# Kernel tuning notes

Hardware: AMD Instinct MI355X
Metric: run time of the kernel (lower is better)

## Reference

```python
import jax, jax.numpy as jnp
import numpy as np

T = 2048
HIDDEN = 4096
NH = 32        # query heads
NKV = 8        # kv heads
G = NH // NKV  # GQA group size
D = 128        # head_dim (== v_head_dim)
ROPE_BASE = 1000000.0


def setup_inputs() -> dict:
    key = jax.random.key(0)
    ks = jax.random.split(key, 8)
    s = 0.02
    return {
        "positions": jnp.arange(T, dtype=jnp.int32),
        "hidden_states": jax.random.normal(ks[0], (T, HIDDEN), dtype=jnp.float32),
        "Wq": jax.random.normal(ks[1], (HIDDEN, NH * D), dtype=jnp.float32) * s,
        "bq": jnp.zeros((NH * D,), dtype=jnp.float32),
        "Wk": jax.random.normal(ks[2], (HIDDEN, NKV * D), dtype=jnp.float32) * s,
        "bk": jnp.zeros((NKV * D,), dtype=jnp.float32),
        "Wv": jax.random.normal(ks[3], (HIDDEN, NKV * D), dtype=jnp.float32) * s,
        "bv": jnp.zeros((NKV * D,), dtype=jnp.float32),
        "Wo": jax.random.normal(ks[4], (NH * D, HIDDEN), dtype=jnp.float32) * s,
    }


def _rope(positions, x):
    # neox-style rotary, full rotary_dim = D
    half = D // 2
    inv_freq = 1.0 / (ROPE_BASE ** (jnp.arange(0, half, dtype=jnp.float32) / half))
    freqs = positions.astype(jnp.float32)[:, None] * inv_freq[None, :]  # [T, half]
    cos = jnp.cos(freqs)[:, None, :]  # [T, 1, half]
    sin = jnp.sin(freqs)[:, None, :]
    x1, x2 = x[..., :half], x[..., half:]
    return jnp.concatenate([x1 * cos - x2 * sin, x2 * cos + x1 * sin], axis=-1)


def reference(positions, hidden_states, Wq, bq, Wk, bk, Wv, bv, Wo):
    q = (hidden_states @ Wq + bq).reshape(T, NH, D)
    k = (hidden_states @ Wk + bk).reshape(T, NKV, D)
    v = (hidden_states @ Wv + bv).reshape(T, NKV, D)
    q = _rope(positions, q)
    k = _rope(positions, k)

    scale = D ** -0.5
    qg = q.reshape(T, NKV, G, D)
    # scores: [NKV, G, T(query), S(key)]
    scores = jnp.einsum("tkgd,skd->kgts", qg, k) * scale
    causal = positions[:, None] >= positions[None, :]  # [T, S]
    scores = jnp.where(causal[None, None, :, :], scores, jnp.finfo(scores.dtype).min)
    probs = jax.nn.softmax(scores, axis=-1)
    attn = jnp.einsum("kgts,skd->tkgd", probs, v).reshape(T, NH * D)

    output = attn @ Wo
    kv_fused = jnp.stack([k, v], axis=0)  # [2, T, NKV, D]
    return output, kv_fused
```

## Files before the change

### kernel.cpp

```cpp
#include <hip/hip_runtime.h>
#include <stdint.h>

#define T_SEQ 2048
#define HIDDEN_DIM 4096
#define NH 32
#define NKV 8
#define HD 128
#define QKV_N 6144

typedef unsigned short u16;
typedef __attribute__((__ext_vector_type__(8))) __bf16 bf16x8;
typedef __attribute__((__ext_vector_type__(4))) float f32x4;

__device__ __forceinline__ float exp2_fast(float x) {
    return __builtin_amdgcn_exp2f(x);
}

__device__ __forceinline__ u16 f2bf(float f) {
    union { float f; unsigned u; } x; x.f = f;
    unsigned u = x.u;
    unsigned r = u + 0x7FFFu + ((u >> 16) & 1u);
    return (u16)(r >> 16);
}
__device__ __forceinline__ float bf2f(u16 h) {
    union { unsigned u; float f; } x; x.u = ((unsigned)h) << 16;
    return x.f;
}

__device__ __forceinline__ void gl_lds16(const u16* g, u16* l) {
    __builtin_amdgcn_global_load_lds((__attribute__((address_space(1))) void*)g,
                                     (__attribute__((address_space(3))) void*)l,
                                     16, 0, 0);
}

#define BAR()                                  \
    {                                          \
        asm volatile("" ::: "memory");         \
        __builtin_amdgcn_s_barrier();          \
        asm volatile("" ::: "memory");         \
    }

template <int N>
__device__ __forceinline__ void vmwait() {
    if constexpr (N == 0) asm volatile("s_waitcnt vmcnt(0)" ::: "memory");
    else if constexpr (N == 3) asm volatile("s_waitcnt vmcnt(3)" ::: "memory");
    else if constexpr (N == 4) asm volatile("s_waitcnt vmcnt(4)" ::: "memory");
    else if constexpr (N == 6) asm volatile("s_waitcnt vmcnt(6)" ::: "memory");
    else if constexpr (N == 8) asm volatile("s_waitcnt vmcnt(8)" ::: "memory");
}

__global__ __launch_bounds__(256) void cast_f32_bf16(const float* __restrict__ in,
                                                     u16* __restrict__ out, int n4) {
    int i = blockIdx.x * 256 + threadIdx.x;
    if (i < n4) {
        float4 v = ((const float4*)in)[i];
        uint2 o;
        o.x = (unsigned)f2bf(v.x) | ((unsigned)f2bf(v.y) << 16);
        o.y = (unsigned)f2bf(v.z) | ((unsigned)f2bf(v.w) << 16);
        ((uint2*)out)[i] = o;
    }
}

__global__ __launch_bounds__(256) void transpose_cast(const float* __restrict__ W,
                                                      u16* __restrict__ Wt, int R, int C) {
    __shared__ float tile[32][33];
    int c0 = blockIdx.x * 32, r0 = blockIdx.y * 32;
    int tx = threadIdx.x & 31;
    int ty = threadIdx.x >> 5;
#pragma unroll
    for (int i = 0; i < 32; i += 8)
        tile[ty + i][tx] = W[(size_t)(r0 + ty + i) * C + c0 + tx];
    __syncthreads();
#pragma unroll
    for (int i = 0; i < 32; i += 8)
        Wt[(size_t)(c0 + ty + i) * R + r0 + tx] = f2bf(tile[tx][ty + i]);
}

__global__ __launch_bounds__(256) void concat_bias(const float* __restrict__ bq,
                                                   const float* __restrict__ bk,
                                                   const float* __restrict__ bv,
                                                   float* __restrict__ out) {
    int i = blockIdx.x * 256 + threadIdx.x;
    if (i < 4096) out[i] = bq[i];
    else if (i < 5120) out[i] = bk[i - 4096];
    else if (i < 6144) out[i] = bv[i - 5120];
}

#define STAGE(SL, S)                                                                         \
    {                                                                                        \
        const size_t ko_ = (size_t)(S) * 32;                                                 \
        _Pragma("unroll") for (int c_ = 0; c_ < ACALLS; ++c_)                                \
            gl_lds16(Ast + ko_ + (size_t)(c_ * 128) * K, &As[SL][c_ * 4096 + wave * 512]);   \
        _Pragma("unroll") for (int c_ = 0; c_ < BFULL; ++c_)                                 \
            gl_lds16(Bst + ko_ + (size_t)(c_ * 128) * K, &Bs[SL][c_ * 4096 + wave * 512]);   \
        if (BHALF) gl_lds16(BstH + ko_, &Bs[SL][BFULL * 4096 + (wave & 3) * 512]);           \
    }

#define REGION(SLOT, NSLOT, CA, CB, NA, NB, RN)                                              \
    {                                                                                        \
        if (RN) {                                                                            \
            _Pragma("unroll") for (int n_ = 0; n_ < NF; ++n_)                                \
                NB[n_] = *(const bf16x8*)&Bs[NSLOT][boff[n_]];                               \
            _Pragma("unroll") for (int m_ = 0; m_ < MF; ++m_)                                \
                NA[m_] = *(const bf16x8*)&As[NSLOT][aoff[m_]];                               \
        }                                                                                    \
        __builtin_amdgcn_s_setprio(1);                                                       \
        _Pragma("unroll") for (int m_ = 0; m_ < MF; ++m_)                                    \
            _Pragma("unroll") for (int n_ = 0; n_ < NF; ++n_)                                \
                acc[m_][n_] = __builtin_amdgcn_mfma_f32_16x16x32_bf16(CA[m_], CB[n_],        \
                                                                      acc[m_][n_], 0, 0, 0); \
        __builtin_amdgcn_s_setprio(0);                                                       \
    }

#define KSTEP(S, SLOT, STG, VMW, RN, CA, CB, NA, NB)          \
    {                                                         \
        if (STG) STAGE((((SLOT) + 3) & 3), (S) + 3)           \
        vmwait<VMW>();                                        \
        BAR();                                                \
        REGION(SLOT, (((SLOT) + 1) & 3), CA, CB, NA, NB, RN)  \
        BAR();                                                \
    }

template <int MF, int NF, int ACALLS, int BFULL, int BHALF, int BF16_OUT, int HAS_BIAS>
__global__ __launch_bounds__(512, 2) void gemm_ph(const u16* __restrict__ A,
                                                  const u16* __restrict__ Bt,
                                                  const float* __restrict__ bias,
                                                  void* __restrict__ Cv,
                                                  int M, int N, int K) {
    constexpr int BM = MF * 32;
    constexpr int BN = NF * 64;
    constexpr int LPS = ACALLS + BFULL + BHALF;
    __shared__ alignas(16) u16 As[4][BM * 32];
    __shared__ alignas(16) u16 Bs[4][BN * 32];
    const int tid = threadIdx.x;
    const int wave = tid >> 6;
    const int lane = tid & 63;
    const int l15 = lane & 15;
    const int quad = lane >> 4;
    const int wr = wave >> 2;
    const int wc = wave & 3;

    const int nbn = N / BN;
    const int q8 = (int)gridDim.x >> 3;
    const int wg = blockIdx.x;
    const int swz = (wg & 7) * q8 + (wg >> 3);
    const int m0 = (swz / nbn) * BM;
    const int n0 = (swz % nbn) * BN;

    const int srow = tid >> 2;
    const int schunk = (tid & 3) ^ ((tid >> 3) & 3);
    const u16* Ast = A + (size_t)(m0 + srow) * K + schunk * 8;
    const u16* Bst = Bt + (size_t)(n0 + srow) * K + schunk * 8;
    const int srowH = (tid & 255) >> 2;
    const u16* BstH = Bt + (size_t)(n0 + BFULL * 128 + srowH) * K + schunk * 8;

    int aoff[MF], boff[NF];
#pragma unroll
    for (int m = 0; m < MF; ++m) {
        int row = wr * (MF * 16) + m * 16 + l15;
        aoff[m] = row * 32 + ((quad ^ ((row >> 1) & 3)) << 3);
    }
#pragma unroll
    for (int n = 0; n < NF; ++n) {
        int row = wc * (NF * 16) + n * 16 + l15;
        boff[n] = row * 32 + ((quad ^ ((row >> 1) & 3)) << 3);
    }

    bf16x8 fA0[MF], fB0[NF], fA1[MF], fB1[NF];
    f32x4 acc[MF][NF] = {};
    const int NS = K >> 5;

    STAGE(0, 0) STAGE(1, 1) STAGE(2, 2)
    vmwait<LPS>();
    BAR();
#pragma unroll
    for (int n = 0; n < NF; ++n) fB0[n] = *(const bf16x8*)&Bs[0][boff[n]];
#pragma unroll
    for (int m = 0; m < MF; ++m) fA0[m] = *(const bf16x8*)&As[0][aoff[m]];

#pragma unroll 1
    for (int s = 0; s < NS - 4; s += 4) {
        KSTEP(s, 0, 1, 2 * LPS, 1, fA0, fB0, fA1, fB1)
        KSTEP(s + 1, 1, 1, 2 * LPS, 1, fA1, fB1, fA0, fB0)
        KSTEP(s + 2, 2, 1, 2 * LPS, 1, fA0, fB0, fA1, fB1)
        KSTEP(s + 3, 3, 1, 2 * LPS, 1, fA1, fB1, fA0, fB0)
    }
    {
        const int s = NS - 4;
        KSTEP(s, 0, 1, 2 * LPS, 1, fA0, fB0, fA1, fB1)
        KSTEP(s + 1, 1, 0, LPS, 1, fA1, fB1, fA0, fB0)
        KSTEP(s + 2, 2, 0, 0, 1, fA0, fB0, fA1, fB1)
        KSTEP(s + 3, 3, 0, 0, 0, fA1, fB1, fA0, fB0)
    }

#pragma unroll
    for (int m = 0; m < MF; ++m) {
        const int row = m0 + wr * (MF * 16) + m * 16 + quad * 4;
#pragma unroll
        for (int n = 0; n < NF; ++n) {
            const int col = n0 + wc * (NF * 16) + n * 16 + l15;
            float b = HAS_BIAS ? bias[col] : 0.f;
#pragma unroll
            for (int r = 0; r < 4; ++r) {
                float v = acc[m][n][r] + b;
                if (BF16_OUT) ((u16*)Cv)[(size_t)(row + r) * N + col] = f2bf(v);
                else ((float*)Cv)[(size_t)(row + r) * N + col] = v;
            }
        }
    }
}

__global__ __launch_bounds__(256) void rope_kernel(const int* __restrict__ positions,
                                                   const u16* __restrict__ qkv,
                                                   u16* __restrict__ qh,
                                                   u16* __restrict__ kh,
                                                   u16* __restrict__ vt,
                                                   float* __restrict__ kv_out) {
    const int t = blockIdx.x;
    const float pos = (float)positions[t];
    const size_t rowbase = (size_t)t * QKV_N;
    const float nlog = -13.815510557964274f / 64.f;
    const float KZ = 0.08838834764831845f * 1.4426950408889634f;
    for (int col = threadIdx.x; col < QKV_N; col += 256) {
        if (col < 4096) {
            int hh = col >> 7, d = col & 127, j = d & 63;
            float ang = pos * __expf((float)j * nlog);
            float cs = cosf(ang), sn = sinf(ang);
            size_t base = rowbase + (size_t)(col & ~127);
            float x1 = bf2f(qkv[base + j]);
            float x2 = bf2f(qkv[base + 64 + j]);
            float v = (d < 64) ? (x1 * cs - x2 * sn) : (x2 * cs + x1 * sn);
            qh[((size_t)hh * T_SEQ + t) * HD + d] = f2bf(v * KZ);
        } else if (col < 5120) {
            int lc = col - 4096, hh = lc >> 7, d = lc & 127, j = d & 63;
            float ang = pos * __expf((float)j * nlog);
            float cs = cosf(ang), sn = sinf(ang);
            size_t base = rowbase + 4096 + (size_t)hh * 128;
            float x1 = bf2f(qkv[base + j]);
            float x2 = bf2f(qkv[base + 64 + j]);
            float v = (d < 64) ? (x1 * cs - x2 * sn) : (x2 * cs + x1 * sn);
            kh[((size_t)hh * T_SEQ + t) * HD + d] = f2bf(v);
            kv_out[((size_t)t * NKV + hh) * HD + d] = v;
        } else {
            int lc = col - 5120, hh = lc >> 7, d = lc & 127;
            float v = bf2f(qkv[rowbase + 5120 + (size_t)hh * 128 + d]);
            vt[((size_t)hh * HD + d) * T_SEQ + t] = f2bf(v);
            kv_out[(((size_t)T_SEQ + t) * NKV + hh) * HD + d] = v;
        }
    }
}

#define KS_STRIDE 136
#define VS_STRIDE 72
#define PS_STRIDE 72

__global__ __launch_bounds__(256) void attn_kernel(const u16* __restrict__ Qh,
                                                   const u16* __restrict__ Kh,
                                                   const u16* __restrict__ Vt,
                                                   u16* __restrict__ attn_out) {
    __shared__ alignas(16) u16 Ks[64 * KS_STRIDE];
    __shared__ alignas(16) u16 Vs[128 * VS_STRIDE];
    __shared__ alignas(16) u16 Ps[4][32 * PS_STRIDE];

    const int h = blockIdx.y;
    const int x = blockIdx.x;
    const int zig = (x & 1) ? ((x - 1) >> 1) : (15 - (x >> 1));
    const int qb = (h < 16) ? zig : (15 - zig);
    const int tid = threadIdx.x;
    const int wave = tid >> 6;
    const int lane = tid & 63;
    const int l15 = lane & 15;
    const int quad = lane >> 4;
    const int kvh = h >> 2;
    const int wrow0 = qb * 128 + wave * 32;

    const u16* Qp = Qh + ((size_t)h * T_SEQ + wrow0) * HD;
    const u16* Kp = Kh + (size_t)kvh * T_SEQ * HD;
    const u16* Vp = Vt + (size_t)kvh * HD * T_SEQ;

    bf16x8 aQ[2][4];
#pragma unroll
    for (int i = 0; i < 2; ++i)
#pragma unroll
        for (int kb = 0; kb < 4; ++kb)
            aQ[i][kb] = *(const bf16x8*)&Qp[(size_t)(i * 16 + l15) * HD + kb * 32 + quad * 8];

    bf16x8 ones;
#pragma unroll
    for (int z = 0; z < 8; ++z) ones[z] = (__bf16)1.0f;

    f32x4 acc[2][8] = {};
    f32x4 accl[2] = {};

    const int n_tiles = 2 * qb + 2;

    const int krow = tid >> 4;
    const int kcol = (tid & 15) * 8;
    const int vrow = tid >> 3;
    const int vcol = (tid & 7) * 8;

#pragma unroll 1
    for (int t = 0; t < n_tiles; ++t) {
        const int s0 = t * 64;
        __syncthreads();
#pragma unroll
        for (int rep = 0; rep < 4; ++rep) {
            int r = krow + rep * 16;
            *(uint4*)&Ks[r * KS_STRIDE + kcol] =
                *(const uint4*)&Kp[(size_t)(s0 + r) * HD + kcol];
        }
#pragma unroll
        for (int rep = 0; rep < 4; ++rep) {
            int d = vrow + rep * 32;
            *(uint4*)&Vs[d * VS_STRIDE + vcol] =
                *(const uint4*)&Vp[(size_t)d * T_SEQ + s0 + vcol];
        }
        __syncthreads();

        if (s0 <= wrow0 + 31) {
            f32x4 sc[2][4];
#pragma unroll
            for (int j = 0; j < 4; ++j) {
                f32x4 sa = {}, sb = {};
#pragma unroll
                for (int kb = 0; kb < 4; ++kb) {
                    bf16x8 bK = *(const bf16x8*)&Ks[(j * 16 + l15) * KS_STRIDE + kb * 32 + quad * 8];
                    sa = __builtin_amdgcn_mfma_f32_16x16x32_bf16(aQ[0][kb], bK, sa, 0, 0, 0);
                    sb = __builtin_amdgcn_mfma_f32_16x16x32_bf16(aQ[1][kb], bK, sb, 0, 0, 0);
                }
                sc[0][j] = sa;
                sc[1][j] = sb;
            }
#pragma unroll
            for (int i = 0; i < 2; ++i)
#pragma unroll
                for (int r = 0; r < 4; ++r) {
                    int t_idx = wrow0 + i * 16 + quad * 4 + r;
#pragma unroll
                    for (int j = 0; j < 4; ++j) {
                        int s_idx = s0 + j * 16 + l15;
                        float z = (s_idx > t_idx) ? -1e30f : sc[i][j][r];
                        float p = exp2_fast(z);
                        Ps[wave][(i * 16 + quad * 4 + r) * PS_STRIDE + j * 16 + l15] = f2bf(p);
                    }
                }
            bf16x8 aP[2][2];
#pragma unroll
            for (int i = 0; i < 2; ++i)
#pragma unroll
                for (int k2 = 0; k2 < 2; ++k2)
                    aP[i][k2] = *(const bf16x8*)&Ps[wave][(i * 16 + l15) * PS_STRIDE + k2 * 32 + quad * 8];
#pragma unroll
            for (int o = 0; o < 8; ++o) {
                bf16x8 bV0 = *(const bf16x8*)&Vs[(o * 16 + l15) * VS_STRIDE + quad * 8];
                bf16x8 bV1 = *(const bf16x8*)&Vs[(o * 16 + l15) * VS_STRIDE + 32 + quad * 8];
#pragma unroll
                for (int i = 0; i < 2; ++i) {
                    acc[i][o] = __builtin_amdgcn_mfma_f32_16x16x32_bf16(aP[i][0], bV0, acc[i][o], 0, 0, 0);
                    acc[i][o] = __builtin_amdgcn_mfma_f32_16x16x32_bf16(aP[i][1], bV1, acc[i][o], 0, 0, 0);
                }
            }
#pragma unroll
            for (int i = 0; i < 2; ++i) {
                accl[i] = __builtin_amdgcn_mfma_f32_16x16x32_bf16(aP[i][0], ones, accl[i], 0, 0, 0);
                accl[i] = __builtin_amdgcn_mfma_f32_16x16x32_bf16(aP[i][1], ones, accl[i], 0, 0, 0);
            }
        }
    }

#pragma unroll
    for (int i = 0; i < 2; ++i)
#pragma unroll
        for (int r = 0; r < 4; ++r) {
            float inv = 1.f / accl[i][r];
            int t_idx = wrow0 + i * 16 + quad * 4 + r;
#pragma unroll
            for (int o = 0; o < 8; ++o)
                attn_out[(size_t)t_idx * (NH * HD) + h * HD + o * 16 + l15] =
                    f2bf(acc[i][o][r] * inv);
        }
}

extern "C" void kernel_launch(void* const* d_in, const int* in_sizes, int n_in,
                              void* d_out, int out_size, void* d_ws, size_t ws_size,
                              hipStream_t stream) {
    const int* positions = (const int*)d_in[0];
    const float* hidden = (const float*)d_in[1];
    const float* Wq = (const float*)d_in[2];
    const float* bq = (const float*)d_in[3];
    const float* Wk = (const float*)d_in[4];
    const float* bk = (const float*)d_in[5];
    const float* Wv = (const float*)d_in[6];
    const float* bv = (const float*)d_in[7];
    const float* Wo = (const float*)d_in[8];

    char* ws = (char*)d_ws;
    u16* hs_bf   = (u16*)(ws + 0);
    u16* attnbuf = (u16*)(ws + 0);
    u16* wqkvT   = (u16*)(ws + 16777216);
    u16* woT     = (u16*)(ws + 16777216);
    u16* qkvbuf  = (u16*)(ws + 67108864);
    u16* qbuf    = (u16*)(ws + 92274688);
    u16* kbuf    = (u16*)(ws + 109051904);
    u16* vtbuf   = (u16*)(ws + 113246208);
    float* biasb = (float*)(ws + 117440512);

    float* out0 = (float*)d_out;
    float* kvout = out0 + (size_t)T_SEQ * HIDDEN_DIM;

    cast_f32_bf16<<<dim3((T_SEQ * HIDDEN_DIM / 4 + 255) / 256), dim3(256), 0, stream>>>(
        hidden, hs_bf, T_SEQ * HIDDEN_DIM / 4);
    transpose_cast<<<dim3(128, 128), dim3(256), 0, stream>>>(Wq, wqkvT, HIDDEN_DIM, 4096);
    transpose_cast<<<dim3(32, 128), dim3(256), 0, stream>>>(Wk, wqkvT + (size_t)4096 * HIDDEN_DIM, HIDDEN_DIM, 1024);
    transpose_cast<<<dim3(32, 128), dim3(256), 0, stream>>>(Wv, wqkvT + (size_t)5120 * HIDDEN_DIM, HIDDEN_DIM, 1024);
    concat_bias<<<dim3(24), dim3(256), 0, stream>>>(bq, bk, bv, biasb);

    gemm_ph<8, 3, 2, 1, 1, 1, 1><<<dim3((T_SEQ / 256) * (QKV_N / 192)), dim3(512), 0, stream>>>(
        hs_bf, wqkvT, biasb, qkvbuf, T_SEQ, QKV_N, HIDDEN_DIM);

    transpose_cast<<<dim3(128, 128), dim3(256), 0, stream>>>(Wo, woT, NH * HD, HIDDEN_DIM);

    rope_kernel<<<dim3(T_SEQ), dim3(256), 0, stream>>>(positions, qkvbuf, qbuf, kbuf, vtbuf, kvout);

    attn_kernel<<<dim3(16, NH), dim3(256), 0, stream>>>(qbuf, kbuf, vtbuf, attnbuf);

    gemm_ph<4, 4, 1, 2, 0, 0, 0><<<dim3((T_SEQ / 128) * (HIDDEN_DIM / 256)), dim3(512), 0, stream>>>(
        attnbuf, woT, nullptr, out0, T_SEQ, HIDDEN_DIM, NH * HD);
}
```

Measured before the change: 539.7 us.

## Add two-phase QKV GEMM kernel and vectorize weight transpose-cast

Adds a dedicated 256x192 GEMM for the QKV projection. Each k-step is split into two MFMA phases, with global-to-LDS prefetch issued between them and fragment loads done without cross-step register double buffering, aiming to cut register pressure and overlap loads with compute. The transpose_cast kernel moves to 64x64 tiles with float4 loads and 16-byte bf16 stores to reduce memory transactions in the weight conversion. The extra barriers per k-step and the changed wait counts could add stalls or affect correctness of the pipeline.

```diff
diff --git a/kernel.cpp b/kernel.cpp
--- a/kernel.cpp
+++ b/kernel.cpp
@@ -63,17 +63,30 @@
 
 __global__ __launch_bounds__(256) void transpose_cast(const float* __restrict__ W,
                                                       u16* __restrict__ Wt, int R, int C) {
-    __shared__ float tile[32][33];
-    int c0 = blockIdx.x * 32, r0 = blockIdx.y * 32;
-    int tx = threadIdx.x & 31;
-    int ty = threadIdx.x >> 5;
-#pragma unroll
-    for (int i = 0; i < 32; i += 8)
-        tile[ty + i][tx] = W[(size_t)(r0 + ty + i) * C + c0 + tx];
+    __shared__ float tile[64][65];
+    const int tid = threadIdx.x;
+    const int c0 = blockIdx.x * 64, r0 = blockIdx.y * 64;
+    const int lr = tid >> 4;
+    const int lc4 = tid & 15;
+#pragma unroll
+    for (int i = 0; i < 4; ++i) {
+        float4 v = *(const float4*)&W[(size_t)(r0 + lr + 16 * i) * C + c0 + lc4 * 4];
+        tile[lr + 16 * i][lc4 * 4 + 0] = v.x;
+        tile[lr + 16 * i][lc4 * 4 + 1] = v.y;
+        tile[lr + 16 * i][lc4 * 4 + 2] = v.z;
+        tile[lr + 16 * i][lc4 * 4 + 3] = v.w;
+    }
     __syncthreads();
-#pragma unroll
-    for (int i = 0; i < 32; i += 8)
-        Wt[(size_t)(c0 + ty + i) * R + r0 + tx] = f2bf(tile[tx][ty + i]);
+    const int rr0 = (tid & 7) * 8;
+    const int cc = tid >> 3;
+#pragma unroll
+    for (int i = 0; i < 2; ++i) {
+        int c = cc + 32 * i;
+        u16 tmp[8];
+#pragma unroll
+        for (int j = 0; j < 8; ++j) tmp[j] = f2bf(tile[rr0 + j][c]);
+        *(uint4*)&Wt[(size_t)(c0 + c) * R + r0 + rr0] = *(const uint4*)tmp;
+    }
 }
 
 __global__ __launch_bounds__(256) void concat_bias(const float* __restrict__ bq,
@@ -84,6 +97,135 @@
     if (i < 4096) out[i] = bq[i];
     else if (i < 5120) out[i] = bk[i - 4096];
     else if (i < 6144) out[i] = bv[i - 5120];
+}
+
+#define KSTEP_2P(S, SLOT, STG, VMW)                                                          \
+    {                                                                                        \
+        bf16x8 bf_[3], af_[4];                                                               \
+        _Pragma("unroll") for (int n = 0; n < 3; ++n)                                        \
+            bf_[n] = *(const bf16x8*)&Bs[SLOT][boff[n]];                                     \
+        _Pragma("unroll") for (int m = 0; m < 4; ++m)                                        \
+            af_[m] = *(const bf16x8*)&As[SLOT][aoff[m]];                                     \
+        if (STG) {                                                                           \
+            gl_lds16(Ast + (size_t)((S) + 3) * 32, &As[((SLOT) + 3) & 3][ldsS0]);            \
+            gl_lds16(Ast + (size_t)((S) + 3) * 32 + rowK128, &As[((SLOT) + 3) & 3][ldsS1]);  \
+        }                                                                                    \
+        BAR();                                                                               \
+        __builtin_amdgcn_s_setprio(1);                                                       \
+        _Pragma("unroll") for (int m = 0; m < 4; ++m)                                        \
+            _Pragma("unroll") for (int n = 0; n < 3; ++n)                                    \
+                acc[m][n] = __builtin_amdgcn_mfma_f32_16x16x32_bf16(af_[m], bf_[n],          \
+                                                                    acc[m][n], 0, 0, 0);     \
+        __builtin_amdgcn_s_setprio(0);                                                       \
+        BAR();                                                                               \
+        _Pragma("unroll") for (int m = 0; m < 4; ++m)                                        \
+            af_[m] = *(const bf16x8*)&As[SLOT][aoff[4 + m]];                                 \
+        if (STG) {                                                                           \
+            gl_lds16(Bst + (size_t)((S) + 3) * 32, &Bs[((SLOT) + 3) & 3][ldsB0]);            \
+            if (tid < 256)                                                                   \
+                gl_lds16(BstH + (size_t)((S) + 3) * 32, &Bs[((SLOT) + 3) & 3][ldsB2]);       \
+        }                                                                                    \
+        BAR();                                                                               \
+        __builtin_amdgcn_s_setprio(1);                                                       \
+        _Pragma("unroll") for (int m = 0; m < 4; ++m)                                        \
+            _Pragma("unroll") for (int n = 0; n < 3; ++n)                                    \
+                acc[4 + m][n] = __builtin_amdgcn_mfma_f32_16x16x32_bf16(af_[m], bf_[n],      \
+                                                                        acc[4 + m][n],       \
+                                                                        0, 0, 0);            \
+        __builtin_amdgcn_s_setprio(0);                                                       \
+        asm volatile("s_waitcnt vmcnt(" #VMW ")" ::: "memory");                              \
+        BAR();                                                                               \
+    }
+
+template <int BF16_OUT, int HAS_BIAS>
+__global__ __launch_bounds__(512, 2) void gemm256(const u16* __restrict__ A,
+                                                  const u16* __restrict__ Bt,
+                                                  const float* __restrict__ bias,
+                                                  void* __restrict__ Cv,
+                                                  int M, int N, int K) {
+    __shared__ alignas(16) u16 As[4][256 * 32];
+    __shared__ alignas(16) u16 Bs[4][192 * 32];
+    const int tid = threadIdx.x;
+    const int wave = tid >> 6;
+    const int lane = tid & 63;
+    const int l15 = lane & 15;
+    const int quad = lane >> 4;
+    const int wr = wave >> 2;
+    const int wc = wave & 3;
+
+    const int nbn = N / 192;
+    const int q8 = (int)gridDim.x >> 3;
+    const int wg = blockIdx.x;
+    const int swz = (wg & 7) * q8 + (wg >> 3);
+    const int m0 = (swz / nbn) * 256;
+    const int n0 = (swz % nbn) * 192;
+
+    const int srow = tid >> 2;
+    const int schunk = (tid & 3) ^ ((tid >> 3) & 3);
+    const u16* Ast = A + (size_t)(m0 + srow) * K + schunk * 8;
+    const u16* Bst = Bt + (size_t)(n0 + srow) * K + schunk * 8;
+    const u16* BstH = Bt + (size_t)(n0 + 128 + srow) * K + schunk * 8;
+    const size_t rowK128 = (size_t)128 * K;
+    const int ldsS0 = wave * 512;
+    const int ldsS1 = 4096 + wave * 512;
+    const int ldsB0 = wave * 512;
+    const int ldsB2 = 4096 + wave * 512;
+
+    int aoff[8], boff[3];
+#pragma unroll
+    for (int m = 0; m < 8; ++m) {
+        int row = wr * 128 + m * 16 + l15;
+        aoff[m] = row * 32 + ((quad ^ ((row >> 1) & 3)) << 3);
+    }
+#pragma unroll
+    for (int n = 0; n < 3; ++n) {
+        int row = wc * 48 + n * 16 + l15;
+        boff[n] = row * 32 + ((quad ^ ((row >> 1) & 3)) << 3);
+    }
+
+    f32x4 acc[8][3] = {};
+    const int NS = K >> 5;
+
+#pragma unroll
+    for (int s = 0; s < 3; ++s) {
+        gl_lds16(Ast + (size_t)s * 32, &As[s][ldsS0]);
+        gl_lds16(Ast + (size_t)s * 32 + rowK128, &As[s][ldsS1]);
+        gl_lds16(Bst + (size_t)s * 32, &Bs[s][ldsB0]);
+        if (tid < 256) gl_lds16(BstH + (size_t)s * 32, &Bs[s][ldsB2]);
+    }
+    asm volatile("s_waitcnt vmcnt(6)" ::: "memory");
+    BAR();
+
+#pragma unroll 1
+    for (int s = 0; s < NS - 4; s += 4) {
+        KSTEP_2P(s, 0, 1, 6)
+        KSTEP_2P(s + 1, 1, 1, 6)
+        KSTEP_2P(s + 2, 2, 1, 6)
+        KSTEP_2P(s + 3, 3, 1, 6)
+    }
+    {
+        const int s = NS - 4;
+        KSTEP_2P(s, 0, 1, 6)
+        KSTEP_2P(s + 1, 1, 0, 6)
+        KSTEP_2P(s + 2, 2, 0, 0)
+        KSTEP_2P(s + 3, 3, 0, 0)
+    }
+
+#pragma unroll
+    for (int m = 0; m < 8; ++m) {
+        const int row = m0 + wr * 128 + m * 16 + quad * 4;
+#pragma unroll
+        for (int n = 0; n < 3; ++n) {
+            const int col = n0 + wc * 48 + n * 16 + l15;
+            float b = HAS_BIAS ? bias[col] : 0.f;
+#pragma unroll
+            for (int r = 0; r < 4; ++r) {
+                float v = acc[m][n][r] + b;
+                if (BF16_OUT) ((u16*)Cv)[(size_t)(row + r) * N + col] = f2bf(v);
+                else ((float*)Cv)[(size_t)(row + r) * N + col] = v;
+            }
+        }
+    }
 }
 
 #define STAGE(SL, S)                                                                         \
@@ -112,7 +254,7 @@
         __builtin_amdgcn_s_setprio(0);                                                       \
     }
 
-#define KSTEP(S, SLOT, STG, VMW, RN, CA, CB, NA, NB)          \
+#define KSTEP_RA(S, SLOT, STG, VMW, RN, CA, CB, NA, NB)       \
     {                                                         \
         if (STG) STAGE((((SLOT) + 3) & 3), (S) + 3)           \
         vmwait<VMW>();                                        \
@@ -180,17 +322,17 @@
 
 #pragma unroll 1
     for (int s = 0; s < NS - 4; s += 4) {
-        KSTEP(s, 0, 1, 2 * LPS, 1, fA0, fB0, fA1, fB1)
-        KSTEP(s + 1, 1, 1, 2 * LPS, 1, fA1, fB1, fA0, fB0)
-        KSTEP(s + 2, 2, 1, 2 * LPS, 1, fA0, fB0, fA1, fB1)
-        KSTEP(s + 3, 3, 1, 2 * LPS, 1, fA1, fB1, fA0, fB0)
+        KSTEP_RA(s, 0, 1, 2 * LPS, 1, fA0, fB0, fA1, fB1)
+        KSTEP_RA(s + 1, 1, 1, 2 * LPS, 1, fA1, fB1, fA0, fB0)
+        KSTEP_RA(s + 2, 2, 1, 2 * LPS, 1, fA0, fB0, fA1, fB1)
+        KSTEP_RA(s + 3, 3, 1, 2 * LPS, 1, fA1, fB1, fA0, fB0)
     }
     {
         const int s = NS - 4;
-        KSTEP(s, 0, 1, 2 * LPS, 1, fA0, fB0, fA1, fB1)
-        KSTEP(s + 1, 1, 0, LPS, 1, fA1, fB1, fA0, fB0)
-        KSTEP(s + 2, 2, 0, 0, 1, fA0, fB0, fA1, fB1)
-        KSTEP(s + 3, 3, 0, 0, 0, fA1, fB1, fA0, fB0)
+        KSTEP_RA(s, 0, 1, 2 * LPS, 1, fA0, fB0, fA1, fB1)
+        KSTEP_RA(s + 1, 1, 0, LPS, 1, fA1, fB1, fA0, fB0)
+        KSTEP_RA(s + 2, 2, 0, 0, 1, fA0, fB0, fA1, fB1)
+        KSTEP_RA(s + 3, 3, 0, 0, 0, fA1, fB1, fA0, fB0)
     }
 
 #pragma unroll
@@ -410,15 +552,15 @@
 
     cast_f32_bf16<<<dim3((T_SEQ * HIDDEN_DIM / 4 + 255) / 256), dim3(256), 0, stream>>>(
         hidden, hs_bf, T_SEQ * HIDDEN_DIM / 4);
-    transpose_cast<<<dim3(128, 128), dim3(256), 0, stream>>>(Wq, wqkvT, HIDDEN_DIM, 4096);
-    transpose_cast<<<dim3(32, 128), dim3(256), 0, stream>>>(Wk, wqkvT + (size_t)4096 * HIDDEN_DIM, HIDDEN_DIM, 1024);
-    transpose_cast<<<dim3(32, 128), dim3(256), 0, stream>>>(Wv, wqkvT + (size_t)5120 * HIDDEN_DIM, HIDDEN_DIM, 1024);
+    transpose_cast<<<dim3(64, 64), dim3(256), 0, stream>>>(Wq, wqkvT, HIDDEN_DIM, 4096);
+    transpose_cast<<<dim3(16, 64), dim3(256), 0, stream>>>(Wk, wqkvT + (size_t)4096 * HIDDEN_DIM, HIDDEN_DIM, 1024);
+    transpose_cast<<<dim3(16, 64), dim3(256), 0, stream>>>(Wv, wqkvT + (size_t)5120 * HIDDEN_DIM, HIDDEN_DIM, 1024);
     concat_bias<<<dim3(24), dim3(256), 0, stream>>>(bq, bk, bv, biasb);
 
-    gemm_ph<8, 3, 2, 1, 1, 1, 1><<<dim3((T_SEQ / 256) * (QKV_N / 192)), dim3(512), 0, stream>>>(
+    gemm256<1, 1><<<dim3((T_SEQ / 256) * (QKV_N / 192)), dim3(512), 0, stream>>>(
         hs_bf, wqkvT, biasb, qkvbuf, T_SEQ, QKV_N, HIDDEN_DIM);
 
-    transpose_cast<<<dim3(128, 128), dim3(256), 0, stream>>>(Wo, woT, NH * HD, HIDDEN_DIM);
+    transpose_cast<<<dim3(64, 64), dim3(256), 0, stream>>>(Wo, woT, NH * HD, HIDDEN_DIM);
 
     rope_kernel<<<dim3(T_SEQ), dim3(256), 0, stream>>>(positions, qkvbuf, qbuf, kbuf, vtbuf, kvout);
 
```

Measured after the change: 528.1 us. -2.2%, faster.
